# Performance work log

Hardware: AMD Instinct MI355X
Metric: run time of the kernel (lower is better)

The kernel has to match this reference:

```python
import jax, jax.numpy as jnp
import numpy as np

N_NODES = 100000
N_EDGES = 1600000
F_IN, HID, N_CLS = 128, 64, 40


def gcn_conv(x, src, dst, W, b, n_nodes):
    # x: [N, Fin] -> [N, Fout]; edges already include self-loops.
    h = x @ W  # [N, Fout]
    ones = jnp.ones_like(src, dtype=h.dtype)
    deg = jax.ops.segment_sum(ones, dst, num_segments=n_nodes)  # [N]
    dinv = jnp.where(deg > 0, jax.lax.rsqrt(deg), 0.0)
    norm = dinv[src] * dinv[dst]  # [E]
    msg = h[src] * norm[:, None]  # gather + scale
    out = jax.ops.segment_sum(msg, dst, num_segments=n_nodes)  # scatter-sum
    return out + b


def setup_inputs() -> dict:
    key = jax.random.key(0)
    ks = jax.random.split(key, 8)
    x = jax.random.normal(ks[0], (N_NODES, F_IN), dtype=jnp.float32)
    edge_index = jax.random.randint(ks[1], (2, N_EDGES), 0, N_NODES, dtype=jnp.int64)

    def glorot(k, fi, fo):
        s = float(np.sqrt(6.0 / (fi + fo)))
        return jax.random.uniform(k, (fi, fo), jnp.float32, -s, s)

    return {
        "x": x,
        "edge_index": edge_index,
        "W1": glorot(ks[2], F_IN, HID), "b1": jnp.zeros((HID,), jnp.float32),
        "W2": glorot(ks[3], HID, HID), "b2": jnp.zeros((HID,), jnp.float32),
        "W3": glorot(ks[4], HID, N_CLS), "b3": jnp.zeros((N_CLS,), jnp.float32),
    }


def reference(x, edge_index, W1, b1, W2, b2, W3, b3):
    n = x.shape[0]
    loop = jnp.arange(n, dtype=edge_index.dtype)
    src = jnp.concatenate([edge_index[0], loop])  # add self-loops
    dst = jnp.concatenate([edge_index[1], loop])
    # layer 1..3: GCNConv -> relu -> dropout(eval: identity)
    h = jax.nn.relu(gcn_conv(x, src, dst, W1, b1, n))
    h = jax.nn.relu(gcn_conv(h, src, dst, W2, b2, n))
    h = jax.nn.relu(gcn_conv(h, src, dst, W3, b3, n))
    return jax.nn.log_softmax(h, axis=1)
```

## Files before the change

kernel.cpp:

```cpp
#include <hip/hip_runtime.h>
#include <math.h>

typedef _Float16 half8   __attribute__((ext_vector_type(8)));
typedef float    float4v __attribute__((ext_vector_type(4)));

#define CAP 6144

static __device__ __forceinline__ unsigned short f32_to_f16u(float f) {
    _Float16 h = (_Float16)f;
    return __builtin_bit_cast(unsigned short, h);
}


__global__ __launch_bounds__(256) void bin_edges(
    const int* __restrict__ src, const int* __restrict__ dst,
    int* __restrict__ bcur, unsigned int* __restrict__ bint, int E, int NB)
{
    __shared__ int h[512];
    __shared__ int rbase[512];
    const int tid = threadIdx.x;
    h[tid] = 0; h[tid + 256] = 0;
    __syncthreads();
    const int eb = blockIdx.x * 4096 + tid;
    int d[16], sr[16];
    #pragma unroll
    for (int k = 0; k < 16; ++k) {
        int i = eb + k * 256;
        if (i < E) {
            d[k] = dst[i]; sr[k] = src[i];
            atomicAdd(&h[d[k] >> 8], 1);
        } else d[k] = -1;
    }
    __syncthreads();
    for (int j = tid; j < NB; j += 256) {
        int c = h[j];
        rbase[j] = c ? atomicAdd(&bcur[j], c) : 0;
        h[j] = 0;
    }
    __syncthreads();
    #pragma unroll
    for (int k = 0; k < 16; ++k) {
        if (d[k] >= 0) {
            int bkt = d[k] >> 8;
            int pos = rbase[bkt] + atomicAdd(&h[bkt], 1);
            if (pos < CAP)
                bint[(size_t)bkt * CAP + pos] =
                    ((unsigned int)sr[k] << 8) | (unsigned int)(d[k] & 255);
        }
    }
}


__global__ __launch_bounds__(256) void build_csr(
    const unsigned int* __restrict__ bint, const int* __restrict__ bcur,
    int2* __restrict__ rp2, float* __restrict__ dinv, int* __restrict__ es, int n)
{
    __shared__ int cnt[256];
    __shared__ int sc[256];
    __shared__ int cur[256];
    const int b = blockIdx.x, tid = threadIdx.x;
    int total = bcur[b]; if (total > CAP) total = CAP;
    const unsigned int* bp = bint + (size_t)b * CAP;
    int* ep = es + (size_t)b * CAP;
    const int base = b * CAP;

    cnt[tid] = 0;
    __syncthreads();
    for (int i = tid; i < total; i += 256)
        atomicAdd(&cnt[bp[i] & 255], 1);
    __syncthreads();

    int v = cnt[tid];
    sc[tid] = v;
    __syncthreads();
    for (int off = 1; off < 256; off <<= 1) {
        int x = (tid >= off) ? sc[tid - off] : 0;
        __syncthreads();
        sc[tid] += x;
        __syncthreads();
    }
    int excl = sc[tid] - v;
    int node = (b << 8) + tid;
    if (node < n) {
        rp2[node]  = make_int2(base + excl, base + excl + v);
        dinv[node] = rsqrtf((float)(v + 1));
    }
    cur[tid] = excl;
    __syncthreads();

    for (int i = tid; i < total; i += 256) {
        unsigned int p = bp[i];
        int pos = atomicAdd(&cur[p & 255], 1);
        ep[pos] = (int)(p >> 8);
    }
}


template<int KK, int NT, int STRIDE, int MOUT, bool INF32>
__global__ __launch_bounds__(256) void gemm_t(
    const void* __restrict__ Xin, const float* __restrict__ W,
    const float* __restrict__ dinv, unsigned short* __restrict__ H, int n)
{
    constexpr int KS = KK >> 5;
    __shared__ __align__(16) unsigned short ldsA[4 * KS * 512];
    const int tid = threadIdx.x;
    const int n0  = blockIdx.x * 64;
    const int wv   = tid >> 6;
    const int lane = tid & 63;
    const int q8 = (lane >> 4) << 3, mc = lane & 15;

    half8 bf[NT * KS];
    #pragma unroll
    for (int u = 0; u < NT; ++u)
        #pragma unroll
        for (int s = 0; s < KS; ++s) {
            const int col = (u << 4) + mc;
            #pragma unroll
            for (int j = 0; j < 8; ++j)
                bf[u * KS + s][j] = (col < MOUT)
                    ? (_Float16)W[((s << 5) + q8 + j) * MOUT + col] : (_Float16)0;
        }

    {
        const int rl = tid >> 3;
        const int kl = tid & 7;
        #pragma unroll
        for (int rb = 0; rb < 64; rb += 32) {
            int r = rl + rb;
            int node = n0 + r;
            int t = r >> 4, m = r & 15;
            #pragma unroll
            for (int kq8 = 0; kq8 < (KK >> 2); kq8 += 8) {
                int k0 = (kl + kq8) << 2;
                unsigned short h[4] = {0, 0, 0, 0};
                if (node < n) {
                    if (INF32) {
                        const float* xp = (const float*)Xin + (size_t)node * KK + k0;
                        float4v v = *(const float4v*)xp;
                        #pragma unroll
                        for (int i = 0; i < 4; ++i) h[i] = f32_to_f16u(v[i]);
                    } else {
                        const unsigned int* ap =
                            (const unsigned int*)Xin + (((size_t)node * KK + k0) >> 1);
                        uint2 v = *(const uint2*)ap;
                        h[0] = (unsigned short)(v.x & 0xffff);
                        h[1] = (unsigned short)(v.x >> 16);
                        h[2] = (unsigned short)(v.y & 0xffff);
                        h[3] = (unsigned short)(v.y >> 16);
                    }
                }
                int s = k0 >> 5, q = (k0 >> 3) & 3, j0 = k0 & 7;
                int lds_lane = (q << 4) | m;
                unsigned short* p = &ldsA[((t * KS + s) << 9) + (lds_lane << 3) + j0];
                unsigned int lo = (unsigned int)h[0] | ((unsigned int)h[1] << 16);
                unsigned int hi = (unsigned int)h[2] | ((unsigned int)h[3] << 16);
                *(uint2*)p = make_uint2(lo, hi);
            }
        }
    }

    __syncthreads();

    float4v acc[NT];
    #pragma unroll
    for (int u = 0; u < NT; ++u) acc[u] = (float4v){0.f, 0.f, 0.f, 0.f};

    #pragma unroll
    for (int s = 0; s < KS; ++s) {
        half8 a = *(const half8*)&ldsA[((wv * KS + s) << 9) + (lane << 3)];
        #pragma unroll
        for (int u = 0; u < NT; ++u)
            acc[u] = __builtin_amdgcn_mfma_f32_16x16x32_f16(a, bf[u * KS + s], acc[u], 0, 0, 0);
    }

    const int quad = lane >> 4;
    #pragma unroll
    for (int reg = 0; reg < 4; ++reg) {
        int node = n0 + (wv << 4) + (quad << 2) + reg;
        if (node >= n) continue;
        float dv = dinv[node];
        #pragma unroll
        for (int u = 0; u < NT; ++u) {
            int col = (u << 4) + mc;
            if (col < MOUT)
                H[(size_t)node * STRIDE + col] = f32_to_f16u(acc[u][reg] * dv);
        }
    }
}


template<int MOUT, int ROWU4>
__global__ __launch_bounds__(256) void gather_t(
    const int2* __restrict__ rp2, const int* __restrict__ es,
    const unsigned short* __restrict__ H, const float* __restrict__ dinv,
    const float* __restrict__ bias, unsigned short* __restrict__ Aout, int n)
{
    const int lane   = threadIdx.x & 63;
    const int half   = lane >> 5;
    const int lane32 = lane & 31;
    const int slot   = (lane >> 3) & 3;
    const int c8     = lane & 7;
    const bool act   = c8 < ROWU4;
    const uint4* H4  = (const uint4*)H;

    float bi[8];
    #pragma unroll
    for (int i = 0; i < 8; ++i) bi[i] = bias[(c8 << 3) + i];

    const half8 hz = {(_Float16)0, (_Float16)0, (_Float16)0, (_Float16)0,
                      (_Float16)0, (_Float16)0, (_Float16)0, (_Float16)0};

    const int TW2 = (int)(gridDim.x << 3);
    for (int nb = (((int)blockIdx.x << 2) + ((int)threadIdx.x >> 6)) << 1; nb < n; nb += TW2) {
        const int node = nb + half;
        const int2 e = rp2[node];
        const float dv = dinv[node];

        half8 hacc = hz;
        if (slot == 0 && act)
            hacc = __builtin_bit_cast(half8, H4[(size_t)node * ROWU4 + c8]);

        for (int cb = e.x; cb < e.y; cb += 32) {
            const int rem = e.y - cb;
            int eidx = cb + lane32; if (eidx > e.y - 1) eidx = e.y - 1;
            const int ei = es[eidx];
            #pragma unroll
            for (int j = 0; j < 8; ++j) {
                const int idx = (j << 2) + slot;
                const int s = __shfl(ei, (half << 5) + idx, 64);
                if (idx < rem && act)
                    hacc = hacc + __builtin_bit_cast(half8, H4[(size_t)s * ROWU4 + c8]);
            }
        }

        #pragma unroll
        for (int step = 8; step <= 16; step <<= 1) {
            uint4 u = __builtin_bit_cast(uint4, hacc);
            uint4 o;
            o.x = __shfl_xor(u.x, step, 64);
            o.y = __shfl_xor(u.y, step, 64);
            o.z = __shfl_xor(u.z, step, 64);
            o.w = __shfl_xor(u.w, step, 64);
            hacc = hacc + __builtin_bit_cast(half8, o);
        }

        if (slot == 0) {
            unsigned short o[8];
            #pragma unroll
            for (int i = 0; i < 8; ++i)
                o[i] = f32_to_f16u(fmaxf((float)hacc[i] * dv + bi[i], 0.0f));
            uint4 w;
            w.x = (unsigned int)o[0] | ((unsigned int)o[1] << 16);
            w.y = (unsigned int)o[2] | ((unsigned int)o[3] << 16);
            w.z = (unsigned int)o[4] | ((unsigned int)o[5] << 16);
            w.w = (unsigned int)o[6] | ((unsigned int)o[7] << 16);
            ((uint4*)Aout)[(size_t)node * 8 + c8] = w;
        }
    }
}


template<int MOUT, int ROWU4>
__global__ __launch_bounds__(256) void gather_softmax(
    const int2* __restrict__ rp2, const int* __restrict__ es,
    const unsigned short* __restrict__ H, const float* __restrict__ dinv,
    const float* __restrict__ bias, float* __restrict__ out, int n)
{
    const int lane   = threadIdx.x & 63;
    const int half   = lane >> 5;
    const int lane32 = lane & 31;
    const int slot   = (lane >> 3) & 3;
    const int c8     = lane & 7;
    const bool act   = c8 < ROWU4;
    const uint4* H4  = (const uint4*)H;

    float bi[8];
    #pragma unroll
    for (int i = 0; i < 8; ++i) {
        int col = (c8 << 3) + i;
        bi[i] = (col < MOUT) ? bias[col] : 0.0f;
    }

    const half8 hz = {(_Float16)0, (_Float16)0, (_Float16)0, (_Float16)0,
                      (_Float16)0, (_Float16)0, (_Float16)0, (_Float16)0};

    const int TW2 = (int)(gridDim.x << 3);
    for (int nb = (((int)blockIdx.x << 2) + ((int)threadIdx.x >> 6)) << 1; nb < n; nb += TW2) {
        const int node = nb + half;
        const int2 e = rp2[node];
        const float dv = dinv[node];

        half8 hacc = hz;
        if (slot == 0 && act)
            hacc = __builtin_bit_cast(half8, H4[(size_t)node * ROWU4 + c8]);

        for (int cb = e.x; cb < e.y; cb += 32) {
            const int rem = e.y - cb;
            int eidx = cb + lane32; if (eidx > e.y - 1) eidx = e.y - 1;
            const int ei = es[eidx];
            #pragma unroll
            for (int j = 0; j < 8; ++j) {
                const int idx = (j << 2) + slot;
                const int s = __shfl(ei, (half << 5) + idx, 64);
                if (idx < rem && act)
                    hacc = hacc + __builtin_bit_cast(half8, H4[(size_t)s * ROWU4 + c8]);
            }
        }

        #pragma unroll
        for (int step = 8; step <= 16; step <<= 1) {
            uint4 u = __builtin_bit_cast(uint4, hacc);
            uint4 o;
            o.x = __shfl_xor(u.x, step, 64);
            o.y = __shfl_xor(u.y, step, 64);
            o.z = __shfl_xor(u.z, step, 64);
            o.w = __shfl_xor(u.w, step, 64);
            hacc = hacc + __builtin_bit_cast(half8, o);
        }

        float z[8]; float m = -INFINITY;
        #pragma unroll
        for (int i = 0; i < 8; ++i) {
            int col = (c8 << 3) + i;
            z[i] = (col < MOUT && act) ? fmaxf((float)hacc[i] * dv + bi[i], 0.0f)
                                       : -INFINITY;
            m = fmaxf(m, z[i]);
        }
        m = fmaxf(m, __shfl_xor(m, 1, 64));
        m = fmaxf(m, __shfl_xor(m, 2, 64));
        m = fmaxf(m, __shfl_xor(m, 4, 64));
        float s = 0.0f;
        #pragma unroll
        for (int i = 0; i < 8; ++i) s += expf(z[i] - m);
        s += __shfl_xor(s, 1, 64);
        s += __shfl_xor(s, 2, 64);
        s += __shfl_xor(s, 4, 64);
        float ls = logf(s) + m;
        if (slot == 0 && c8 < (MOUT + 7) / 8) {
            float* op = out + (size_t)node * MOUT + (c8 << 3);
            float4v o0 = {z[0] - ls, z[1] - ls, z[2] - ls, z[3] - ls};
            float4v o1 = {z[4] - ls, z[5] - ls, z[6] - ls, z[7] - ls};
            *(float4v*)op = o0;
            *(float4v*)(op + 4) = o1;
        }
    }
}


extern "C" void kernel_launch(void* const* d_in, const int* in_sizes, int n_in,
                              void* d_out, int out_size, void* d_ws, size_t ws_size,
                              hipStream_t stream)
{
    const float* x  = (const float*)d_in[0];
    const int*   ei = (const int*)  d_in[1];
    const float* W1 = (const float*)d_in[2];
    const float* b1 = (const float*)d_in[3];
    const float* W2 = (const float*)d_in[4];
    const float* b2 = (const float*)d_in[5];
    const float* W3 = (const float*)d_in[6];
    const float* b3 = (const float*)d_in[7];

    const int F_IN = 128;
    const int n = in_sizes[0] / F_IN;
    const int E = in_sizes[1] / 2;
    const int* src = ei;
    const int* dst = ei + E;
    float* out = (float*)d_out;

    const int NB = (n + 255) >> 8;

    auto align = [](size_t v) { return (v + 255) & ~(size_t)255; };
    char* w = (char*)d_ws;
    size_t off = 0;
    float*          dinv = (float*)(w + off);          off = align(off + (size_t)n * 4);
    unsigned short* H1   = (unsigned short*)(w + off); off = align(off + (size_t)n * 64 * 2);
    unsigned short* A    = (unsigned short*)(w + off); off = align(off + (size_t)n * 64 * 2);
    unsigned short* H3   = (unsigned short*)(w + off); off = align(off + (size_t)n * 40 * 2);
    int2*           rp2  = (int2*)(w + off);           off = align(off + (size_t)n * 8);
    int*            es   = (int*)(w + off);            off = align(off + (size_t)NB * CAP * 4);
    unsigned int*   bint = (unsigned int*)(w + off);   off = align(off + (size_t)NB * CAP * 4);
    int*            bcur = (int*)(w + off);            off = align(off + (size_t)512 * 4);
    unsigned short* H2   = H1;

    const int BLK = 256;
    auto cdiv = [](int a, int b) { return (a + b - 1) / b; };
    const int EB = cdiv(E, 4096);
    const int GB = cdiv(n, 64);
    const int GG = 2048;

    hipMemsetAsync(bcur, 0, (size_t)512 * 4, stream);
    bin_edges<<<EB, BLK, 0, stream>>>(src, dst, bcur, bint, E, NB);
    build_csr<<<NB, BLK, 0, stream>>>(bint, bcur, rp2, dinv, es, n);

    gemm_t<128, 4, 64, 64, true><<<GB, BLK, 0, stream>>>(x, W1, dinv, H1, n);
    gather_t<64, 8><<<GG, BLK, 0, stream>>>(rp2, es, H1, dinv, b1, A, n);

    gemm_t<64, 4, 64, 64, false><<<GB, BLK, 0, stream>>>(A, W2, dinv, H2, n);
    gather_t<64, 8><<<GG, BLK, 0, stream>>>(rp2, es, H2, dinv, b2, A, n);

    gemm_t<64, 3, 40, 40, false><<<GB, BLK, 0, stream>>>(A, W3, dinv, H3, n);
    gather_softmax<40, 5><<<GG, BLK, 0, stream>>>(rp2, es, H3, dinv, b3, out, n);
}
```

Measured before the change: 278.0 us.

## Shrink CSR buckets to 196 nodes, fix bin grid, vectorize fp16 GEMM loads

Edge binning now uses buckets of 196 destination nodes instead of 256. The bucket index comes from a multiply-shift division, so build_csr runs about 511 blocks, which gives better coverage of the CUs, and the per-bucket capacity drops to 4096. bin_edges switches to a fixed 512-block grid that processes contiguous chunks with strided loops instead of holding 16 edges per thread in registers. The fp16-input GEMM path now loads 8 halves with one 16-byte load per thread instead of several 8-byte loads. Risks are bucket overflow past CAP for skewed graphs and correctness of the magic-constant division for large node ids.

```diff
diff --git a/kernel.cpp b/kernel.cpp
--- a/kernel.cpp
+++ b/kernel.cpp
@@ -4,11 +4,17 @@
 typedef _Float16 half8   __attribute__((ext_vector_type(8)));
 typedef float    float4v __attribute__((ext_vector_type(4)));
 
-#define CAP 6144
+#define NPB   196
+#define CAP   4096
+#define DIVM  342393ull
 
 static __device__ __forceinline__ unsigned short f32_to_f16u(float f) {
     _Float16 h = (_Float16)f;
     return __builtin_bit_cast(unsigned short, h);
+}
+
+static __device__ __forceinline__ int bkt_of(int d) {
+    return (int)(((unsigned long long)(unsigned)d * DIVM) >> 26);
 }
 
 
@@ -21,32 +27,30 @@
     const int tid = threadIdx.x;
     h[tid] = 0; h[tid + 256] = 0;
     __syncthreads();
-    const int eb = blockIdx.x * 4096 + tid;
-    int d[16], sr[16];
-    #pragma unroll
-    for (int k = 0; k < 16; ++k) {
-        int i = eb + k * 256;
-        if (i < E) {
-            d[k] = dst[i]; sr[k] = src[i];
-            atomicAdd(&h[d[k] >> 8], 1);
-        } else d[k] = -1;
-    }
-    __syncthreads();
+
+    const int chunk = (E + (int)gridDim.x - 1) / (int)gridDim.x;
+    const int base  = (int)blockIdx.x * chunk;
+    int end = base + chunk; if (end > E) end = E;
+
+    for (int i = base + tid; i < end; i += 256)
+        atomicAdd(&h[bkt_of(dst[i])], 1);
+    __syncthreads();
+
     for (int j = tid; j < NB; j += 256) {
         int c = h[j];
         rbase[j] = c ? atomicAdd(&bcur[j], c) : 0;
         h[j] = 0;
     }
     __syncthreads();
-    #pragma unroll
-    for (int k = 0; k < 16; ++k) {
-        if (d[k] >= 0) {
-            int bkt = d[k] >> 8;
-            int pos = rbase[bkt] + atomicAdd(&h[bkt], 1);
-            if (pos < CAP)
-                bint[(size_t)bkt * CAP + pos] =
-                    ((unsigned int)sr[k] << 8) | (unsigned int)(d[k] & 255);
-        }
+
+    for (int i = base + tid; i < end; i += 256) {
+        int d = dst[i];
+        int bkt = bkt_of(d);
+        int low = d - bkt * NPB;
+        int pos = rbase[bkt] + atomicAdd(&h[bkt], 1);
+        if (pos < CAP)
+            bint[(size_t)bkt * CAP + pos] =
+                ((unsigned int)src[i] << 8) | (unsigned int)low;
     }
 }
 
@@ -70,7 +74,7 @@
         atomicAdd(&cnt[bp[i] & 255], 1);
     __syncthreads();
 
-    int v = cnt[tid];
+    int v = (tid < NPB) ? cnt[tid] : 0;
     sc[tid] = v;
     __syncthreads();
     for (int off = 1; off < 256; off <<= 1) {
@@ -80,8 +84,8 @@
         __syncthreads();
     }
     int excl = sc[tid] - v;
-    int node = (b << 8) + tid;
-    if (node < n) {
+    int node = b * NPB + tid;
+    if (tid < NPB && node < n) {
         rp2[node]  = make_int2(base + excl, base + excl + v);
         dinv[node] = rsqrtf((float)(v + 1));
     }
@@ -129,32 +133,31 @@
             int r = rl + rb;
             int node = n0 + r;
             int t = r >> 4, m = r & 15;
-            #pragma unroll
-            for (int kq8 = 0; kq8 < (KK >> 2); kq8 += 8) {
-                int k0 = (kl + kq8) << 2;
-                unsigned short h[4] = {0, 0, 0, 0};
-                if (node < n) {
-                    if (INF32) {
+            if (INF32) {
+                #pragma unroll
+                for (int kq8 = 0; kq8 < (KK >> 2); kq8 += 8) {
+                    int k0 = (kl + kq8) << 2;
+                    unsigned short h[4] = {0, 0, 0, 0};
+                    if (node < n) {
                         const float* xp = (const float*)Xin + (size_t)node * KK + k0;
                         float4v v = *(const float4v*)xp;
                         #pragma unroll
                         for (int i = 0; i < 4; ++i) h[i] = f32_to_f16u(v[i]);
-                    } else {
-                        const unsigned int* ap =
-                            (const unsigned int*)Xin + (((size_t)node * KK + k0) >> 1);
-                        uint2 v = *(const uint2*)ap;
-                        h[0] = (unsigned short)(v.x & 0xffff);
-                        h[1] = (unsigned short)(v.x >> 16);
-                        h[2] = (unsigned short)(v.y & 0xffff);
-                        h[3] = (unsigned short)(v.y >> 16);
                     }
+                    int s = k0 >> 5, q = (k0 >> 3) & 3, j0 = k0 & 7;
+                    int lds_lane = (q << 4) | m;
+                    unsigned short* p = &ldsA[((t * KS + s) << 9) + (lds_lane << 3) + j0];
+                    *(uint2*)p = make_uint2((unsigned)h[0] | ((unsigned)h[1] << 16),
+                                            (unsigned)h[2] | ((unsigned)h[3] << 16));
                 }
-                int s = k0 >> 5, q = (k0 >> 3) & 3, j0 = k0 & 7;
-                int lds_lane = (q << 4) | m;
-                unsigned short* p = &ldsA[((t * KS + s) << 9) + (lds_lane << 3) + j0];
-                unsigned int lo = (unsigned int)h[0] | ((unsigned int)h[1] << 16);
-                unsigned int hi = (unsigned int)h[2] | ((unsigned int)h[3] << 16);
-                *(uint2*)p = make_uint2(lo, hi);
+            } else {
+                uint4 v = make_uint4(0, 0, 0, 0);
+                if (node < n)
+                    v = *(const uint4*)((const unsigned short*)Xin + (size_t)node * KK + (kl << 3));
+                int k0 = kl << 3;
+                int s = k0 >> 5, q = (k0 >> 3) & 3;
+                unsigned short* p = &ldsA[((t * KS + s) << 9) + ((((q << 4) | m)) << 3)];
+                *(uint4*)p = v;
             }
         }
     }
@@ -367,7 +370,7 @@
     const int* dst = ei + E;
     float* out = (float*)d_out;
 
-    const int NB = (n + 255) >> 8;
+    const int NB = (n + NPB - 1) / NPB;
 
     auto align = [](size_t v) { return (v + 255) & ~(size_t)255; };
     char* w = (char*)d_ws;
@@ -379,17 +382,16 @@
     int2*           rp2  = (int2*)(w + off);           off = align(off + (size_t)n * 8);
     int*            es   = (int*)(w + off);            off = align(off + (size_t)NB * CAP * 4);
     unsigned int*   bint = (unsigned int*)(w + off);   off = align(off + (size_t)NB * CAP * 4);
-    int*            bcur = (int*)(w + off);            off = align(off + (size_t)512 * 4);
+    int*            bcur = (int*)(w + off);            off = align(off + (size_t)1024 * 4);
     unsigned short* H2   = H1;
 
     const int BLK = 256;
     auto cdiv = [](int a, int b) { return (a + b - 1) / b; };
-    const int EB = cdiv(E, 4096);
     const int GB = cdiv(n, 64);
     const int GG = 2048;
 
-    hipMemsetAsync(bcur, 0, (size_t)512 * 4, stream);
-    bin_edges<<<EB, BLK, 0, stream>>>(src, dst, bcur, bint, E, NB);
+    hipMemsetAsync(bcur, 0, (size_t)1024 * 4, stream);
+    bin_edges<<<512, BLK, 0, stream>>>(src, dst, bcur, bint, E, NB);
     build_csr<<<NB, BLK, 0, stream>>>(bint, bcur, rp2, dinv, es, n);
 
     gemm_t<128, 4, 64, 64, true><<<GB, BLK, 0, stream>>>(x, W1, dinv, H1, n);
```

After: 283.1 us. Within noise of the previous version (+1.8%).
